# Kernel optimization log

Measured on AMD Instinct MI355X. Metric: run time of the kernel, lower is better.

## Reference

```python
import jax, jax.numpy as jnp
import numpy as np

B, N, CIN, COUT, K, E = 2048, 64, 128, 256, 3, 256
EPS = 1e-5


def setup_inputs() -> dict:
    key = jax.random.key(0)
    ks = jax.random.split(key, 8)
    x = jax.random.normal(ks[0], (B, N, CIN), dtype=jnp.float32)
    edge_index = jax.random.randint(ks[1], (2, E), 0, N, dtype=jnp.int32)
    W = jax.random.normal(ks[2], (CIN, COUT), dtype=jnp.float32) / np.sqrt(CIN)
    b_gcn = jnp.zeros((COUT,), jnp.float32)
    w_conv = jax.random.normal(ks[3], (COUT, COUT, K), dtype=jnp.float32) / np.sqrt(COUT * K)
    b_conv = jnp.zeros((COUT,), jnp.float32)
    gamma = jnp.ones((COUT,), jnp.float32)
    beta = jnp.zeros((COUT,), jnp.float32)
    return {"x": x, "W": W, "b_gcn": b_gcn, "w_conv": w_conv, "b_conv": b_conv,
            "gamma": gamma, "beta": beta, "edge_index": edge_index}


def reference(x, W, b_gcn, w_conv, b_conv, gamma, beta, edge_index):
    Bq, Nn, _ = x.shape
    Co = W.shape[1]
    # ---- GCNConv (PyG semantics: xW, add self-loops, symmetric norm, + bias) ----
    src, dst = edge_index[0], edge_index[1]
    loop = jnp.arange(Nn, dtype=edge_index.dtype)
    src2 = jnp.concatenate([src, loop])           # [E+N]
    dst2 = jnp.concatenate([dst, loop])
    deg = jnp.zeros((Nn,), x.dtype).at[dst2].add(1.0)
    dinv = jnp.where(deg > 0, jax.lax.rsqrt(deg), 0.0)
    norm = dinv[src2] * dinv[dst2]                # [E+N]
    xw = jnp.einsum('bnc,co->bno', x, W)          # [B, N, Co]
    msgs = xw[:, src2, :] * norm[None, :, None]   # [B, E+N, Co]
    x_gcn = jnp.zeros((Bq, Nn, Co), x.dtype).at[:, dst2, :].add(msgs) + b_gcn
    # ---- temporal Conv1d over batch_seq axis, shared weights across nodes ----
    xt = x_gcn.transpose(1, 2, 0)                 # [N, Co, B]  (time = batch_seq)
    pad = K // 2
    y = jax.lax.conv_general_dilated(xt, w_conv, (1,), [(pad, pad)],
                                     dimension_numbers=('NCH', 'OIH', 'NCH'))
    y = y + b_conv[None, :, None]                 # [N, Co, B]
    # ---- BatchNorm1d (training-mode batch stats) + ReLU ----
    y = y.transpose(2, 1, 0)                      # [B, Co, N]
    mean = y.mean(axis=(0, 2), keepdims=True)
    var = ((y - mean) ** 2).mean(axis=(0, 2), keepdims=True)
    y = (y - mean) * jax.lax.rsqrt(var + EPS)
    y = gamma[None, :, None] * y + beta[None, :, None]
    y = jax.nn.relu(y)
    # dropout is identity in eval mode
    return y.transpose(0, 2, 1)                   # [B, N, Co]
```

## Files before the change

kernel.cpp:

```cpp
#include <hip/hip_runtime.h>
#include <hip/hip_bf16.h>

typedef __attribute__((ext_vector_type(8))) unsigned short us8;
typedef __attribute__((ext_vector_type(4))) unsigned short us4;
typedef __attribute__((ext_vector_type(8))) short short8;
typedef __attribute__((ext_vector_type(4))) float f32x4;

#define BB 2048
#define NN 64
#define CIN 128
#define CO 256
#define KWIN 3
#define EE 256
#define NE 320
#define EPSBN 1e-5f

static __device__ __forceinline__ void gload_lds16(const unsigned short* g, unsigned short* l) {
    __builtin_amdgcn_global_load_lds(
        (const __attribute__((address_space(1))) unsigned int*)g,
        (__attribute__((address_space(3))) unsigned int*)l,
        16, 0, 0);
}

static __device__ __forceinline__ float bf2f(unsigned short u) {
    return __uint_as_float(((unsigned int)u) << 16);
}

static __device__ __forceinline__ unsigned short f2bfu(float f) {
    unsigned int u = __float_as_uint(f);
    u = (u + 0x7FFFu + ((u >> 16) & 1u)) >> 16;
    return (unsigned short)u;
}

__global__ __launch_bounds__(256) void k_prep(const int* __restrict__ ei,
                                              const float* __restrict__ W,
                                              const float* __restrict__ wconv,
                                              __hip_bfloat16* __restrict__ Ahat,
                                              __hip_bfloat16* __restrict__ Wtf,
                                              __hip_bfloat16* __restrict__ W2f) {
    __shared__ int s_cnt[NN * NN];
    __shared__ int s_deg[NN];
    __shared__ float s_dinv[NN];
    const int t = threadIdx.x;
    if (blockIdx.x == 896) {
        for (int i = t; i < NN * NN; i += 256) s_cnt[i] = 0;
        if (t < NN) s_deg[t] = 0;
        __syncthreads();
        for (int e = t; e < NE; e += 256) {
            int src, dst;
            if (e < EE) { src = ei[e]; dst = ei[EE + e]; }
            else        { src = e - EE; dst = e - EE; }
            atomicAdd(&s_deg[dst], 1);
            atomicAdd(&s_cnt[dst * NN + src], 1);
        }
        __syncthreads();
        if (t < NN) s_dinv[t] = rsqrtf((float)s_deg[t]);
        __syncthreads();
        for (int i = t; i < NN * NN; i += 256) {
            const int n = i >> 6, m = i & 63;
            Ahat[i] = __float2bfloat16((float)s_cnt[i] * s_dinv[m] * s_dinv[n]);
        }
        return;
    }
    const int idx = blockIdx.x * 256 + t;
    if (idx < CO * CIN) {
        const int o16 = idx >> 11, s = (idx >> 9) & 3;
        const int l = (idx >> 3) & 63, e = idx & 7;
        const int o = o16 * 16 + (l & 15);
        const int c = s * 32 + (l >> 4) * 8 + e;
        Wtf[idx] = __float2bfloat16(W[c * CO + o]);
    }
    const int j = idx - CO * CIN;
    if (j >= 0 && j < CO * KWIN * CO) {
        const int o16 = j / 12288, r = j - o16 * 12288;
        const int kc = r >> 9, r2 = r & 511;
        const int l = r2 >> 3, e = r2 & 7;
        const int o = o16 * 16 + (l & 15);
        const int k = kc * 32 + (l >> 4) * 8 + e;
        W2f[j] = __float2bfloat16(wconv[(o * CO + (k & 255)) * KWIN + (k >> 8)]);
    }
}

__global__ __launch_bounds__(256) void k_gcn(const float* __restrict__ x,
                                             const __hip_bfloat16* __restrict__ Ahat_,
                                             const __hip_bfloat16* __restrict__ Wtf_,
                                             const float* __restrict__ bgcn,
                                             __hip_bfloat16* __restrict__ xgcn_) {
    __shared__ __align__(16) unsigned short sx[64 * 128];
    __shared__ __align__(16) unsigned short stm[256 * 64];
    const unsigned short* Ahat = (const unsigned short*)Ahat_;
    const unsigned short* Wtf  = (const unsigned short*)Wtf_;
    unsigned short* xgcn = (unsigned short*)xgcn_;

    const int b = blockIdx.x, tid = threadIdx.x;
    const int lane = tid & 63, wid = tid >> 6;
    const int llo = lane & 15, lhi = lane >> 4;

#pragma unroll
    for (int r = 0; r < 4; ++r) {
        const int f = tid + 256 * r;
        const int m = f >> 4, c0 = (f & 15) * 8;
        const float4* src = (const float4*)(x + ((size_t)b * NN + m) * CIN + c0);
        const float4 v0 = src[0], v1 = src[1];
        unsigned short t8[8] = {f2bfu(v0.x), f2bfu(v0.y), f2bfu(v0.z), f2bfu(v0.w),
                                f2bfu(v1.x), f2bfu(v1.y), f2bfu(v1.z), f2bfu(v1.w)};
        *(us8*)&sx[m * 128 + (c0 ^ ((m & 7) << 3))] = *(const us8*)t8;
    }
    __syncthreads();

    f32x4 acc1[4][4];
#pragma unroll
    for (int p = 0; p < 4; ++p)
#pragma unroll
        for (int q = 0; q < 4; ++q) acc1[p][q] = (f32x4){0.f, 0.f, 0.f, 0.f};
#pragma unroll
    for (int s = 0; s < 4; ++s) {
        const int k0 = s * 32 + lhi * 8;
        short8 af[4], bf[4];
#pragma unroll
        for (int p = 0; p < 4; ++p) {
            const int m = p * 16 + llo;
            af[p] = *(const short8*)&sx[m * 128 + (k0 ^ ((m & 7) << 3))];
        }
#pragma unroll
        for (int q = 0; q < 4; ++q)
            bf[q] = *(const short8*)&Wtf[(((wid * 4 + q) * 4 + s) * 64 + lane) * 8];
#pragma unroll
        for (int p = 0; p < 4; ++p)
#pragma unroll
            for (int q = 0; q < 4; ++q)
                acc1[p][q] = __builtin_amdgcn_mfma_f32_16x16x32_bf16(af[p], bf[q], acc1[p][q], 0, 0, 0);
    }
#pragma unroll
    for (int p = 0; p < 4; ++p)
#pragma unroll
        for (int q = 0; q < 4; ++q) {
            const int o = wid * 64 + q * 16 + llo;
            const int bm = p * 16 + lhi * 4;
            unsigned short t4[4] = {f2bfu(acc1[p][q][0]), f2bfu(acc1[p][q][1]),
                                    f2bfu(acc1[p][q][2]), f2bfu(acc1[p][q][3])};
            *(us4*)&stm[o * 64 + (bm ^ ((o & 7) << 3))] = *(const us4*)t4;
        }

    f32x4 acc2[4][4];
#pragma unroll
    for (int p = 0; p < 4; ++p)
#pragma unroll
        for (int q = 0; q < 4; ++q) acc2[p][q] = (f32x4){0.f, 0.f, 0.f, 0.f};
#pragma unroll
    for (int s = 0; s < 2; ++s) {
        const int k0 = s * 32 + lhi * 8;
        short8 af[4], bf[4];
#pragma unroll
        for (int p = 0; p < 4; ++p) {
            const int n = p * 16 + llo;
            af[p] = *(const short8*)&Ahat[n * 64 + k0];
        }
#pragma unroll
        for (int q = 0; q < 4; ++q) {
            const int o = wid * 64 + q * 16 + llo;
            bf[q] = *(const short8*)&stm[o * 64 + (k0 ^ ((o & 7) << 3))];
        }
#pragma unroll
        for (int p = 0; p < 4; ++p)
#pragma unroll
            for (int q = 0; q < 4; ++q)
                acc2[p][q] = __builtin_amdgcn_mfma_f32_16x16x32_bf16(af[p], bf[q], acc2[p][q], 0, 0, 0);
    }

    float bg[4];
#pragma unroll
    for (int q = 0; q < 4; ++q) bg[q] = bgcn[wid * 64 + q * 16 + llo];
#pragma unroll
    for (int p = 0; p < 4; ++p)
#pragma unroll
        for (int q = 0; q < 4; ++q) {
            const int o = wid * 64 + q * 16 + llo;
#pragma unroll
            for (int reg = 0; reg < 4; ++reg) {
                const int n = p * 16 + lhi * 4 + reg;
                xgcn[((size_t)n * BB + b) * CO + o] = f2bfu(acc2[p][q][reg] + bg[q]);
            }
        }
}

__global__ __launch_bounds__(512, 4) void k_conv(const __hip_bfloat16* __restrict__ xgcn_,
                                                 const __hip_bfloat16* __restrict__ W2f_,
                                                 const float* __restrict__ bconv,
                                                 __hip_bfloat16* __restrict__ y_,
                                                 float* __restrict__ partials) {
    __shared__ __align__(16) unsigned short sA[130 * 256];
    const unsigned short* xgcn = (const unsigned short*)xgcn_;
    const unsigned short* W2f  = (const unsigned short*)W2f_;
    unsigned short* y = (unsigned short*)y_;

    const int tt = blockIdx.x, n = blockIdx.y;
    const int tid = threadIdx.x;
    const int lane = tid & 63, wid = tid >> 6;
    const int t0 = tt * 128;
    const int wm = wid >> 2, wo4 = wid & 3;
    const int wm0 = wm * 64, wo0 = wo4 * 64;
    const int lhi = lane >> 4, llo = lane & 15;

    f32x4 acc[4][4];
#pragma unroll
    for (int p = 0; p < 4; ++p)
#pragma unroll
        for (int q = 0; q < 4; ++q) acc[p][q] = (f32x4){0.f, 0.f, 0.f, 0.f};

    {
        const int rsub = lane >> 5;
        const int g = lane & 31;
        for (int iss = wid; iss < 65; iss += 8) {
            const int r = 2 * iss + rsub;
            int bg = t0 - 1 + r;
            bg = min(max(bg, 0), BB - 1);
            const int col = ((g ^ (r & 7)) << 3);
            gload_lds16(xgcn + ((size_t)n * BB + bg) * CO + col, sA + iss * 512);
        }
    }
    __syncthreads();
    if (tt == 0 || tt == 15) {
        const int zr = (tt == 0) ? 0 : 129;
        if (tid < 32) *(uint4*)&sA[zr * 256 + tid * 8] = make_uint4(0u, 0u, 0u, 0u);
        __syncthreads();
    }

    const unsigned short* bq[4];
#pragma unroll
    for (int q = 0; q < 4; ++q) {
        const int o16 = wo4 * 4 + q;
        bq[q] = W2f + ((size_t)o16 * 24) * 512 + lane * 8;
    }
#pragma unroll 4
    for (int kc = 0; kc < 24; ++kc) {
        const int kk = kc >> 3;
        const int G = (kc & 7) * 4 + lhi;
        short8 af[4], bf[4];
#pragma unroll
        for (int p = 0; p < 4; ++p) {
            const int sr = wm0 + p * 16 + llo + kk;
            af[p] = *(const short8*)&sA[sr * 256 + ((G ^ (sr & 7)) << 3)];
        }
#pragma unroll
        for (int q = 0; q < 4; ++q)
            bf[q] = *(const short8*)(bq[q] + kc * 512);
        __builtin_amdgcn_s_setprio(1);
#pragma unroll
        for (int p = 0; p < 4; ++p)
#pragma unroll
            for (int q = 0; q < 4; ++q)
                acc[p][q] = __builtin_amdgcn_mfma_f32_16x16x32_bf16(af[p], bf[q], acc[p][q], 0, 0, 0);
        __builtin_amdgcn_s_setprio(0);
    }

    float bc[4], s1v[4], s2v[4];
#pragma unroll
    for (int q = 0; q < 4; ++q) {
        bc[q] = bconv[wo0 + q * 16 + llo];
        s1v[q] = 0.f; s2v[q] = 0.f;
    }
#pragma unroll
    for (int p = 0; p < 4; ++p) {
#pragma unroll
        for (int reg = 0; reg < 4; ++reg) {
            const int trow = t0 + wm0 + p * 16 + lhi * 4 + reg;
            unsigned short* dst = y + ((size_t)trow * NN + n) * CO + wo0 + llo;
#pragma unroll
            for (int q = 0; q < 4; ++q) {
                const float v = acc[p][q][reg] + bc[q];
                dst[q * 16] = f2bfu(v);
                s1v[q] += v;
                s2v[q] += v * v;
            }
        }
    }
    __syncthreads();
    float* sred1 = (float*)sA;
    float* sred2 = sred1 + 2048;
    const int rg = wm * 4 + lhi;
#pragma unroll
    for (int q = 0; q < 4; ++q) {
        const int cl = wo0 + q * 16 + llo;
        sred1[rg * 256 + cl] = s1v[q];
        sred2[rg * 256 + cl] = s2v[q];
    }
    __syncthreads();
    if (tid < 256) {
        float a = 0.f, b2 = 0.f;
#pragma unroll
        for (int r = 0; r < 8; ++r) { a += sred1[r * 256 + tid]; b2 += sred2[r * 256 + tid]; }
        float* pb = partials + (size_t)(n * 16 + tt) * 512;
        pb[tid * 2]     = a;
        pb[tid * 2 + 1] = b2;
    }
}

__global__ __launch_bounds__(256) void k_bnstats(const float* __restrict__ partials,
                                                 const float* __restrict__ gamma,
                                                 const float* __restrict__ beta,
                                                 float* __restrict__ scl,
                                                 float* __restrict__ shf) {
    const int o = blockIdx.x, tid = threadIdx.x;
    float s1 = 0.f, s2 = 0.f;
    for (int i = tid; i < 1024; i += 256) {
        const float* p = partials + (size_t)i * 512 + o * 2;
        s1 += p[0]; s2 += p[1];
    }
    __shared__ float r1[256], r2[256];
    r1[tid] = s1; r2[tid] = s2;
    __syncthreads();
    for (int s = 128; s > 0; s >>= 1) {
        if (tid < s) { r1[tid] += r1[tid + s]; r2[tid] += r2[tid + s]; }
        __syncthreads();
    }
    if (tid == 0) {
        const float inv = 1.f / (float)((size_t)BB * NN);
        const float mean = r1[0] * inv;
        const float var  = r2[0] * inv - mean * mean;
        const float sc = gamma[o] * rsqrtf(var + EPSBN);
        scl[o] = sc;
        shf[o] = beta[o] - mean * sc;
    }
}

__global__ __launch_bounds__(256) void k_apply(const unsigned short* __restrict__ y,
                                               float* __restrict__ out,
                                               const float* __restrict__ scl,
                                               const float* __restrict__ shf) {
    __shared__ float ssc[CO], ssh[CO];
    const int tid = threadIdx.x;
    ssc[tid] = scl[tid]; ssh[tid] = shf[tid];
    __syncthreads();
    const size_t total8 = (size_t)BB * NN * CO / 8;
    float4* out4 = (float4*)out;
    for (size_t i = (size_t)blockIdx.x * 256 + tid; i < total8; i += (size_t)gridDim.x * 256) {
        const us8 v = *(const us8*)(y + i * 8);
        const int ob = (int)((i * 8) & (CO - 1));
        float4 r0, r1;
        r0.x = fmaxf(0.f, bf2f(v[0]) * ssc[ob + 0] + ssh[ob + 0]);
        r0.y = fmaxf(0.f, bf2f(v[1]) * ssc[ob + 1] + ssh[ob + 1]);
        r0.z = fmaxf(0.f, bf2f(v[2]) * ssc[ob + 2] + ssh[ob + 2]);
        r0.w = fmaxf(0.f, bf2f(v[3]) * ssc[ob + 3] + ssh[ob + 3]);
        r1.x = fmaxf(0.f, bf2f(v[4]) * ssc[ob + 4] + ssh[ob + 4]);
        r1.y = fmaxf(0.f, bf2f(v[5]) * ssc[ob + 5] + ssh[ob + 5]);
        r1.z = fmaxf(0.f, bf2f(v[6]) * ssc[ob + 6] + ssh[ob + 6]);
        r1.w = fmaxf(0.f, bf2f(v[7]) * ssc[ob + 7] + ssh[ob + 7]);
        out4[i * 2]     = r0;
        out4[i * 2 + 1] = r1;
    }
}

extern "C" void kernel_launch(void* const* d_in, const int* in_sizes, int n_in,
                              void* d_out, int out_size, void* d_ws, size_t ws_size,
                              hipStream_t stream) {
    const float* x     = (const float*)d_in[0];
    const float* W     = (const float*)d_in[1];
    const float* bgcn  = (const float*)d_in[2];
    const float* wconv = (const float*)d_in[3];
    const float* bconv = (const float*)d_in[4];
    const float* gamma = (const float*)d_in[5];
    const float* beta  = (const float*)d_in[6];
    const int*   ei    = (const int*)d_in[7];
    float* out = (float*)d_out;

    char* ws = (char*)d_ws;
    size_t off = 0;
    __hip_bfloat16* xgcn = (__hip_bfloat16*)(ws + off); off += (size_t)BB * NN * CO * 2;
    __hip_bfloat16* ybuf = (__hip_bfloat16*)(ws + off); off += (size_t)BB * NN * CO * 2;
    __hip_bfloat16* W2f  = (__hip_bfloat16*)(ws + off); off += (size_t)CO * KWIN * CO * 2;
    __hip_bfloat16* Ahat = (__hip_bfloat16*)(ws + off); off += (size_t)NN * NN * 2;
    __hip_bfloat16* Wtf  = (__hip_bfloat16*)(ws + off); off += (size_t)CO * CIN * 2;
    float* partials = (float*)(ws + off); off += (size_t)1024 * 512 * 4;
    float* scl = (float*)(ws + off); off += 256 * 4;
    float* shf = (float*)(ws + off); off += 256 * 4;

    k_prep<<<897, 256, 0, stream>>>(ei, W, wconv, Ahat, Wtf, W2f);
    k_gcn<<<BB, 256, 0, stream>>>(x, Ahat, Wtf, bgcn, xgcn);
    k_conv<<<dim3(16, 64), 512, 0, stream>>>(xgcn, W2f, bconv, ybuf, partials);
    k_bnstats<<<256, 256, 0, stream>>>(partials, gamma, beta, scl, shf);
    k_apply<<<2048, 256, 0, stream>>>((const unsigned short*)ybuf, out, scl, shf);
}
```

Before: 143.8 us.

## Stage GCN output in LDS for coalesced stores, switch xgcn layout, nontemporal apply

The GCN kernel now writes its per-batch output tile into shared memory (reusing the input buffers) and then stores it contiguously with 16-byte vector writes. Previously each thread did scattered 2-byte stores into an [N,B,CO] layout. The intermediate layout becomes [B,N,CO], and the conv kernel's gather addresses are changed to match. The apply kernel uses nontemporal loads and stores to avoid polluting the cache with streaming data. This adds an extra barrier and LDS round-trip in k_gcn, and the conv loads now stride across batches by N*CO.

```diff
diff --git a/kernel.cpp b/kernel.cpp
--- a/kernel.cpp
+++ b/kernel.cpp
@@ -86,8 +86,10 @@
                                              const __hip_bfloat16* __restrict__ Wtf_,
                                              const float* __restrict__ bgcn,
                                              __hip_bfloat16* __restrict__ xgcn_) {
-    __shared__ __align__(16) unsigned short sx[64 * 128];
-    __shared__ __align__(16) unsigned short stm[256 * 64];
+    __shared__ __align__(16) char smem[49152];
+    unsigned short* sx   = (unsigned short*)smem;
+    unsigned short* stm  = (unsigned short*)(smem + 16384);
+    unsigned short* sout = (unsigned short*)smem;
     const unsigned short* Ahat = (const unsigned short*)Ahat_;
     const unsigned short* Wtf  = (const unsigned short*)Wtf_;
     unsigned short* xgcn = (unsigned short*)xgcn_;
@@ -167,6 +169,7 @@
             for (int q = 0; q < 4; ++q)
                 acc2[p][q] = __builtin_amdgcn_mfma_f32_16x16x32_bf16(af[p], bf[q], acc2[p][q], 0, 0, 0);
     }
+    __syncthreads();
 
     float bg[4];
 #pragma unroll
@@ -179,9 +182,16 @@
 #pragma unroll
             for (int reg = 0; reg < 4; ++reg) {
                 const int n = p * 16 + lhi * 4 + reg;
-                xgcn[((size_t)n * BB + b) * CO + o] = f2bfu(acc2[p][q][reg] + bg[q]);
+                sout[n * CO + o] = f2bfu(acc2[p][q][reg] + bg[q]);
             }
         }
+    __syncthreads();
+    unsigned short* dst = xgcn + (size_t)b * NN * CO;
+#pragma unroll
+    for (int r = 0; r < 8; ++r) {
+        const int f = tid + 256 * r;
+        *(us8*)(dst + f * 8) = *(const us8*)&sout[f * 8];
+    }
 }
 
 __global__ __launch_bounds__(512, 4) void k_conv(const __hip_bfloat16* __restrict__ xgcn_,
@@ -216,7 +226,7 @@
             int bg = t0 - 1 + r;
             bg = min(max(bg, 0), BB - 1);
             const int col = ((g ^ (r & 7)) << 3);
-            gload_lds16(xgcn + ((size_t)n * BB + bg) * CO + col, sA + iss * 512);
+            gload_lds16(xgcn + ((size_t)bg * NN + n) * CO + col, sA + iss * 512);
         }
     }
     __syncthreads();
@@ -333,21 +343,21 @@
     ssc[tid] = scl[tid]; ssh[tid] = shf[tid];
     __syncthreads();
     const size_t total8 = (size_t)BB * NN * CO / 8;
-    float4* out4 = (float4*)out;
+    f32x4* out4 = (f32x4*)out;
     for (size_t i = (size_t)blockIdx.x * 256 + tid; i < total8; i += (size_t)gridDim.x * 256) {
-        const us8 v = *(const us8*)(y + i * 8);
+        const us8 v = __builtin_nontemporal_load((const us8*)(y + i * 8));
         const int ob = (int)((i * 8) & (CO - 1));
-        float4 r0, r1;
-        r0.x = fmaxf(0.f, bf2f(v[0]) * ssc[ob + 0] + ssh[ob + 0]);
-        r0.y = fmaxf(0.f, bf2f(v[1]) * ssc[ob + 1] + ssh[ob + 1]);
-        r0.z = fmaxf(0.f, bf2f(v[2]) * ssc[ob + 2] + ssh[ob + 2]);
-        r0.w = fmaxf(0.f, bf2f(v[3]) * ssc[ob + 3] + ssh[ob + 3]);
-        r1.x = fmaxf(0.f, bf2f(v[4]) * ssc[ob + 4] + ssh[ob + 4]);
-        r1.y = fmaxf(0.f, bf2f(v[5]) * ssc[ob + 5] + ssh[ob + 5]);
-        r1.z = fmaxf(0.f, bf2f(v[6]) * ssc[ob + 6] + ssh[ob + 6]);
-        r1.w = fmaxf(0.f, bf2f(v[7]) * ssc[ob + 7] + ssh[ob + 7]);
-        out4[i * 2]     = r0;
-        out4[i * 2 + 1] = r1;
+        f32x4 r0, r1;
+        r0[0] = fmaxf(0.f, bf2f(v[0]) * ssc[ob + 0] + ssh[ob + 0]);
+        r0[1] = fmaxf(0.f, bf2f(v[1]) * ssc[ob + 1] + ssh[ob + 1]);
+        r0[2] = fmaxf(0.f, bf2f(v[2]) * ssc[ob + 2] + ssh[ob + 2]);
+        r0[3] = fmaxf(0.f, bf2f(v[3]) * ssc[ob + 3] + ssh[ob + 3]);
+        r1[0] = fmaxf(0.f, bf2f(v[4]) * ssc[ob + 4] + ssh[ob + 4]);
+        r1[1] = fmaxf(0.f, bf2f(v[5]) * ssc[ob + 5] + ssh[ob + 5]);
+        r1[2] = fmaxf(0.f, bf2f(v[6]) * ssc[ob + 6] + ssh[ob + 6]);
+        r1[3] = fmaxf(0.f, bf2f(v[7]) * ssc[ob + 7] + ssh[ob + 7]);
+        __builtin_nontemporal_store(r0, out4 + i * 2);
+        __builtin_nontemporal_store(r1, out4 + i * 2 + 1);
     }
 }
 
```

Result: slower. 164.7 us (+14.6%).
